# Optimization experiments

Measured on AMD Instinct MI355X. Metric: run time of the kernel, lower is better.

Reference implementation:

```python
import jax, jax.numpy as jnp
from jax import lax
import numpy as np

# db4 (Daubechies-4) filters, matching pywt.Wavelet('db4')
L = 8
_REC_LO = np.array([0.23037781330885523, 0.7148465705525415, 0.6308807679295904,
                    -0.02798376941698385, -0.18703481171888114, 0.030841381835986965,
                    0.032883011666982945, -0.010597401784997278], dtype=np.float32)
_DEC_LO = _REC_LO[::-1].copy()
_DEC_HI = (((-1.0) ** (np.arange(L) + 1)) * _REC_LO).astype(np.float32)  # QMF
_REC_HI = _DEC_HI[::-1].copy()
# lax.conv performs correlation, so use reversed filters to get true convolution.
# rev(dec_lo)=rec_lo, rev(dec_hi)=rec_hi and vice versa.
DEC_K = jnp.asarray(np.stack([_DEC_LO[::-1], _DEC_HI[::-1]])[:, None, :])  # (2,1,L)
REC_K = jnp.asarray(np.stack([_REC_LO[::-1], _REC_HI[::-1]])[None, :, :])  # (1,2,L)

ENHANCE_FACTOR = 1.5
DENOISE_THRESHOLD = 0.2


def _dwt_last(x):
    # pywt single-level DWT (mode='symmetric') along last axis.
    # Equivalent to: conv(sym_pad(x, L-1), dec_filter)[valid][1::2]
    xe = jnp.pad(x, ((0, 0), (L - 1, L - 1)), mode='symmetric')[:, 1:]
    y = lax.conv_general_dilated(xe[:, None, :], DEC_K, (2,), 'VALID',
                                 dimension_numbers=('NCH', 'OIH', 'NCH'))
    return y[:, 0], y[:, 1]  # lo, hi, each (M, (S+L-1)//2)


def _idwt_last(lo, hi):
    # pywt single-level IDWT: upsample (lhs_dilation=2), filter, trim L-2 each side.
    c = jnp.stack([lo, hi], axis=1)  # (M, 2, n)
    y = lax.conv_general_dilated(c, REC_K, (1,), [(1, 1)], lhs_dilation=(2,),
                                 dimension_numbers=('NCH', 'OIH', 'NCH'))
    return y[:, 0]  # (M, 2n - L + 2)


def _dwt2(x):
    # x: (N, H, W) -> aa (cA), da (cH), ad (cV), dd (cD)
    N, H, W = x.shape
    lo, hi = _dwt_last(x.reshape(N * H, W))
    Wc = lo.shape[-1]
    lo = lo.reshape(N, H, Wc)
    hi = hi.reshape(N, H, Wc)

    def colwise(a):
        at = a.transpose(0, 2, 1).reshape(N * Wc, H)
        l, h = _dwt_last(at)
        Hc = l.shape[-1]
        return (l.reshape(N, Wc, Hc).transpose(0, 2, 1),
                h.reshape(N, Wc, Hc).transpose(0, 2, 1))

    aa, da = colwise(lo)
    ad, dd = colwise(hi)
    return aa, da, ad, dd


def _idwt2(aa, da, ad, dd):
    N, Hc, Wc = aa.shape

    def colinv(a, d):
        at = a.transpose(0, 2, 1).reshape(N * Wc, Hc)
        dt = d.transpose(0, 2, 1).reshape(N * Wc, Hc)
        r = _idwt_last(at, dt)
        H = r.shape[-1]
        return r.reshape(N, Wc, H).transpose(0, 2, 1)

    lo = colinv(aa, da)
    hi = colinv(ad, dd)
    H = lo.shape[1]
    out = _idwt_last(lo.reshape(N * H, Wc), hi.reshape(N * H, Wc))
    return out.reshape(N, H, -1)


def _soft_enhance(d):
    # enhance then pywt.threshold(..., mode='soft') with per-(image,channel,band) max
    d = d * ENHANCE_FACTOR
    t = DENOISE_THRESHOLD * jnp.max(jnp.abs(d), axis=(-2, -1), keepdims=True)
    return jnp.sign(d) * jnp.maximum(jnp.abs(d) - t, 0.0)


def setup_inputs() -> dict:
    key = jax.random.key(0)
    x = jax.random.normal(key, (32, 3, 510, 510), dtype=jnp.float32)
    return {'x': x}


def reference(x):
    B, C, H, W = x.shape
    z = x.reshape(B * C, H, W)
    a1, h1, v1, d1 = _dwt2(z)
    a2, h2, v2, d2 = _dwt2(a1)
    h2s, v2s, d2s = _soft_enhance(h2), _soft_enhance(v2), _soft_enhance(d2)
    h1s, v1s, d1s = _soft_enhance(h1), _soft_enhance(v1), _soft_enhance(d1)
    a1r = _idwt2(a2, h2s, v2s, d2s)
    out = _idwt2(a1r, h1s, v1s, d1s)
    return out.reshape(B, C, H, W)
```

## Files before the change

kernel.cpp:

```cpp
#include <hip/hip_runtime.h>

__constant__ float c_dec_lo[8] = {
    -0.010597401784997278f, 0.032883011666982945f, 0.030841381835986965f,
    -0.18703481171888114f, -0.02798376941698385f, 0.6308807679295904f,
    0.7148465705525415f, 0.23037781330885523f};
__constant__ float c_dec_hi[8] = {
    -0.23037781330885523f, 0.7148465705525415f, -0.6308807679295904f,
    -0.02798376941698385f, 0.18703481171888114f, 0.030841381835986965f,
    -0.032883011666982945f, -0.010597401784997278f};
__constant__ float c_rec_lo[8] = {
    0.23037781330885523f, 0.7148465705525415f, 0.6308807679295904f,
    -0.02798376941698385f, -0.18703481171888114f, 0.030841381835986965f,
    0.032883011666982945f, -0.010597401784997278f};
__constant__ float c_rec_hi[8] = {
    -0.010597401784997278f, -0.032883011666982945f, 0.030841381835986965f,
    0.18703481171888114f, -0.02798376941698385f, -0.6308807679295904f,
    0.7148465705525415f, -0.23037781330885523f};

__device__ __forceinline__ float soft_enh(float v, float th) {
    float e = 1.5f * v;
    float a = fabsf(e) - th;
    return a > 0.0f ? copysignf(a, e) : 0.0f;
}

#define TB 32
#define TO 64

__global__ __launch_bounds__(256, 8) void fused_dwt2_k(
    const float* __restrict__ x, int S, int Nc, int tiles,
    float* __restrict__ aa, float* __restrict__ da,
    float* __restrict__ ad, float* __restrict__ dd,
    unsigned* __restrict__ mx_da, unsigned* __restrict__ mx_ad,
    unsigned* __restrict__ mx_dd)
{
    int b = blockIdx.x;
    int tx = b % tiles, ty = (b / tiles) % tiles, m = b / (tiles * tiles);
    int jh0 = ty * TB, jw0 = tx * TB;
    int r0 = 2 * jh0 - 6, c0 = 2 * jw0 - 6;
    const float* xm = x + (size_t)m * S * S;

    __shared__ float RB[70][68];

    int tid = threadIdx.x;
    bool colv = (c0 >= 0) && (c0 + 71 < S);

    if (colv) {
        for (int e = tid; e < 560; e += 256) {
            int r = e >> 3, q = e & 7;
            int pr = r0 + r;
            pr = pr < 0 ? -1 - pr : pr;
            pr = pr >= S ? 2 * S - 1 - pr : pr;
            const float* src = xm + (size_t)pr * S + (c0 + 8 * q);
            float f[16];
#pragma unroll
            for (int i = 0; i < 8; ++i) {
                float2 v = *reinterpret_cast<const float2*>(src + 2 * i);
                f[2 * i] = v.x; f[2 * i + 1] = v.y;
            }
            float lo[4], hi[4];
#pragma unroll
            for (int i = 0; i < 4; ++i) {
                float alo = 0.f, ahi = 0.f;
#pragma unroll
                for (int t = 0; t < 8; ++t) {
                    float v = f[2 * i + 7 - t];
                    alo = fmaf(c_dec_lo[t], v, alo);
                    ahi = fmaf(c_dec_hi[t], v, ahi);
                }
                lo[i] = alo; hi[i] = ahi;
            }
            int c4 = 4 * q;
            *reinterpret_cast<float4*>(&RB[r][c4]) = make_float4(lo[0], lo[1], lo[2], lo[3]);
            *reinterpret_cast<float4*>(&RB[r][32 + c4]) = make_float4(hi[0], hi[1], hi[2], hi[3]);
        }
    } else {
        for (int e = tid; e < 70 * 32; e += 256) {
            int r = e >> 5, jj = e & 31;
            int pr = r0 + r;
            pr = pr < 0 ? -1 - pr : pr;
            pr = pr >= S ? 2 * S - 1 - pr : pr;
            const float* row = xm + (size_t)pr * S;
            int pb = c0 + 2 * jj;
            float alo = 0.f, ahi = 0.f;
#pragma unroll
            for (int t = 0; t < 8; ++t) {
                int p = pb + 7 - t;
                p = p < 0 ? -1 - p : p;
                p = p >= S ? 2 * S - 1 - p : p;
                float v = row[p];
                alo = fmaf(c_dec_lo[t], v, alo);
                ahi = fmaf(c_dec_hi[t], v, ahi);
            }
            RB[r][jj] = alo; RB[r][32 + jj] = ahi;
        }
    }
    __syncthreads();

    int jj = tid & 31, g = tid >> 5;
    int jw = jw0 + jj;
    float mh = 0.f, mv = 0.f, md = 0.f;
#pragma unroll
    for (int pass = 0; pass < 2; ++pass) {
        int rbase = 8 * g + 4 * pass;
        float L[10], H[10];
#pragma unroll
        for (int rr = 0; rr < 10; ++rr) {
            L[rr] = RB[rbase + rr][jj];
            H[rr] = RB[rbase + rr][32 + jj];
        }
#pragma unroll
        for (int k = 0; k < 2; ++k) {
            float vaa = 0.f, vda = 0.f, vad = 0.f, vdd = 0.f;
#pragma unroll
            for (int t = 0; t < 8; ++t) {
                float l = L[2 * k + 7 - t];
                float h = H[2 * k + 7 - t];
                vaa = fmaf(c_dec_lo[t], l, vaa);
                vda = fmaf(c_dec_hi[t], l, vda);
                vad = fmaf(c_dec_lo[t], h, vad);
                vdd = fmaf(c_dec_hi[t], h, vdd);
            }
            int jh = jh0 + 4 * g + 2 * pass + k;
            if (jh < Nc && jw < Nc) {
                size_t o = ((size_t)m * Nc + jh) * Nc + jw;
                aa[o] = vaa; da[o] = vda; ad[o] = vad; dd[o] = vdd;
                mh = fmaxf(mh, fabsf(vda));
                mv = fmaxf(mv, fabsf(vad));
                md = fmaxf(md, fabsf(vdd));
            }
        }
    }
#pragma unroll
    for (int off = 32; off; off >>= 1) {
        mh = fmaxf(mh, __shfl_down(mh, off));
        mv = fmaxf(mv, __shfl_down(mv, off));
        md = fmaxf(md, __shfl_down(md, off));
    }
    __shared__ float sm[3][4];
    int wv = tid >> 6, ln = tid & 63;
    if (ln == 0) { sm[0][wv] = mh; sm[1][wv] = mv; sm[2][wv] = md; }
    __syncthreads();
    if (tid == 0) {
        float A = fmaxf(fmaxf(sm[0][0], sm[0][1]), fmaxf(sm[0][2], sm[0][3]));
        float B = fmaxf(fmaxf(sm[1][0], sm[1][1]), fmaxf(sm[1][2], sm[1][3]));
        float C = fmaxf(fmaxf(sm[2][0], sm[2][1]), fmaxf(sm[2][2], sm[2][3]));
        atomicMax(mx_da + m, __float_as_uint(A));
        atomicMax(mx_ad + m, __float_as_uint(B));
        atomicMax(mx_dd + m, __float_as_uint(C));
    }
}

__global__ __launch_bounds__(256, 8) void fused_idwt2_k(
    const float* __restrict__ a, const float* __restrict__ h,
    const float* __restrict__ v, const float* __restrict__ d,
    const unsigned* __restrict__ mxh, const unsigned* __restrict__ mxv,
    const unsigned* __restrict__ mxd,
    int n, int Ho, int tiles, float* __restrict__ out)
{
    int b = blockIdx.x;
    int tx = b % tiles, ty = (b / tiles) % tiles, m = b / (tiles * tiles);
    int i0 = ty * TO, u0 = tx * TO;
    int jr0 = i0 >> 1, jc0 = u0 >> 1;

    __shared__ float LH[TO][71];

    int tid = threadIdx.x;
    float th_h = 0.2f * (1.5f * __uint_as_float(mxh[m]));
    float th_v = 0.2f * (1.5f * __uint_as_float(mxv[m]));
    float th_d = 0.2f * (1.5f * __uint_as_float(mxd[m]));
    const float* am = a + (size_t)m * n * n;
    const float* hm = h + (size_t)m * n * n;
    const float* vm = v + (size_t)m * n * n;
    const float* dm = d + (size_t)m * n * n;

    for (int task = tid; task < 8 * 35; task += 256) {
        int g = task / 35, jc = task % 35;
        int jcg = jc0 + jc; if (jcg > n - 1) jcg = n - 1;
#pragma unroll
        for (int pass = 0; pass < 2; ++pass) {
            int P = 2 * g + pass;
            float acc_lo[4], acc_hi[4];
#pragma unroll
            for (int k = 0; k < 4; ++k) { acc_lo[k] = 0.f; acc_hi[k] = 0.f; }
#pragma unroll
            for (int rl = 0; rl < 5; ++rl) {
                int jr = jr0 + 2 * P + rl; if (jr > n - 1) jr = n - 1;
                size_t o = (size_t)jr * n + jcg;
                float av = am[o];
                float hv = soft_enh(hm[o], th_h);
                float vv = soft_enh(vm[o], th_v);
                float dv = soft_enh(dm[o], th_d);
#pragma unroll
                for (int t = 0; t < 8; ++t) {
                    int k = 2 * rl + t - 6;
                    if (k >= 0 && k < 4) {
                        acc_lo[k] = fmaf(c_rec_lo[t], av, fmaf(c_rec_hi[t], hv, acc_lo[k]));
                        acc_hi[k] = fmaf(c_rec_lo[t], vv, fmaf(c_rec_hi[t], dv, acc_hi[k]));
                    }
                }
            }
#pragma unroll
            for (int k = 0; k < 4; ++k) {
                LH[4 * P + k][jc] = acc_lo[k];
                LH[4 * P + k][35 + jc] = acc_hi[k];
            }
        }
    }
    __syncthreads();

    for (int e = tid; e < TO * TO; e += 256) {
        int il = e >> 6, ul = e & 63;
        int t0 = ul & 1;
        float acc = 0.f;
#pragma unroll
        for (int s = 0; s < 4; ++s) {
            int t = t0 + 2 * s;
            int c = (ul + 6 - t) >> 1;
            acc = fmaf(c_rec_lo[t], LH[il][c], acc);
            acc = fmaf(c_rec_hi[t], LH[il][35 + c], acc);
        }
        int gi = i0 + il, gu = u0 + ul;
        if (gi < Ho && gu < Ho)
            out[((size_t)m * Ho + gi) * Ho + gu] = acc;
    }
}

extern "C" void kernel_launch(void* const* d_in, const int* in_sizes, int n_in,
                              void* d_out, int out_size, void* d_ws, size_t ws_size,
                              hipStream_t stream) {
    const float* x = (const float*)d_in[0];
    float* out = (float*)d_out;
    float* ws = (float*)d_ws;

    const int M = 96, S1 = 510, N1 = 258, N2 = 132;
    const long S_l1 = (long)M * N1 * N1;
    const long S_l2 = (long)M * N2 * N2;

    float* aa1 = ws;
    float* h1  = aa1 + S_l1;
    float* v1  = h1 + S_l1;
    float* d1  = v1 + S_l1;
    float* a1r = d1 + S_l1;
    float* a2  = a1r + S_l1;
    float* h2  = a2 + S_l2;
    float* v2  = h2 + S_l2;
    float* d2  = v2 + S_l2;
    unsigned* th = (unsigned*)(d2 + S_l2);

    long need = 5 * S_l1 + 4 * S_l2 + 576;
    if (ws_size < (size_t)need * sizeof(float)) return;

    unsigned *th_h1 = th, *th_v1 = th + 96, *th_d1 = th + 192;
    unsigned *th_h2 = th + 288, *th_v2 = th + 384, *th_d2 = th + 480;

    hipMemsetAsync(th, 0, 576 * sizeof(unsigned), stream);

    fused_dwt2_k<<<9 * 9 * M, 256, 0, stream>>>(x, S1, N1, 9, aa1, h1, v1, d1,
                                                th_h1, th_v1, th_d1);
    fused_dwt2_k<<<5 * 5 * M, 256, 0, stream>>>(aa1, N1, N2, 5, a2, h2, v2, d2,
                                                th_h2, th_v2, th_d2);
    fused_idwt2_k<<<5 * 5 * M, 256, 0, stream>>>(a2, h2, v2, d2, th_h2, th_v2, th_d2,
                                                 N2, N1, 5, a1r);
    fused_idwt2_k<<<8 * 8 * M, 256, 0, stream>>>(a1r, h1, v1, d1, th_h1, th_v1, th_d1,
                                                 N1, S1, 8, out);
}
```

Measured before the change: 360.7 us.

## Batch global loads up front, reuse idwt column rows, use constexpr filters

```diff
diff --git a/kernel.cpp b/kernel.cpp
--- a/kernel.cpp
+++ b/kernel.cpp
@@ -1,18 +1,18 @@
 #include <hip/hip_runtime.h>
 
-__constant__ float c_dec_lo[8] = {
+__device__ constexpr float DEC_LO[8] = {
     -0.010597401784997278f, 0.032883011666982945f, 0.030841381835986965f,
     -0.18703481171888114f, -0.02798376941698385f, 0.6308807679295904f,
     0.7148465705525415f, 0.23037781330885523f};
-__constant__ float c_dec_hi[8] = {
+__device__ constexpr float DEC_HI[8] = {
     -0.23037781330885523f, 0.7148465705525415f, -0.6308807679295904f,
     -0.02798376941698385f, 0.18703481171888114f, 0.030841381835986965f,
     -0.032883011666982945f, -0.010597401784997278f};
-__constant__ float c_rec_lo[8] = {
+__device__ constexpr float REC_LO[8] = {
     0.23037781330885523f, 0.7148465705525415f, 0.6308807679295904f,
     -0.02798376941698385f, -0.18703481171888114f, 0.030841381835986965f,
     0.032883011666982945f, -0.010597401784997278f};
-__constant__ float c_rec_hi[8] = {
+__device__ constexpr float REC_HI[8] = {
     -0.010597401784997278f, -0.032883011666982945f, 0.030841381835986965f,
     0.18703481171888114f, -0.02798376941698385f, -0.6308807679295904f,
     0.7148465705525415f, -0.23037781330885523f};
@@ -26,7 +26,7 @@
 #define TB 32
 #define TO 64
 
-__global__ __launch_bounds__(256, 8) void fused_dwt2_k(
+__global__ __launch_bounds__(256, 4) void fused_dwt2_k(
     const float* __restrict__ x, int S, int Nc, int tiles,
     float* __restrict__ aa, float* __restrict__ da,
     float* __restrict__ ad, float* __restrict__ dd,
@@ -44,56 +44,75 @@
     int tid = threadIdx.x;
     bool colv = (c0 >= 0) && (c0 + 71 < S);
 
+    int e0 = tid, e1 = tid + 256, e2 = tid + 512;
+    bool has2 = (e2 < 560);
+
+    auto prow = [&](int e) -> const float* {
+        int pr = r0 + (e >> 3);
+        pr = pr < 0 ? -1 - pr : pr;
+        pr = pr >= S ? 2 * S - 1 - pr : pr;
+        return xm + (size_t)pr * S;
+    };
+
+    float f0[16], f1[16], f2[16];
     if (colv) {
-        for (int e = tid; e < 560; e += 256) {
-            int r = e >> 3, q = e & 7;
-            int pr = r0 + r;
-            pr = pr < 0 ? -1 - pr : pr;
-            pr = pr >= S ? 2 * S - 1 - pr : pr;
-            const float* src = xm + (size_t)pr * S + (c0 + 8 * q);
-            float f[16];
+        const float* s0 = prow(e0) + (c0 + 8 * (e0 & 7));
+        const float* s1 = prow(e1) + (c0 + 8 * (e1 & 7));
+#pragma unroll
+        for (int i = 0; i < 8; ++i) {
+            float2 v = *reinterpret_cast<const float2*>(s0 + 2 * i);
+            f0[2 * i] = v.x; f0[2 * i + 1] = v.y;
+        }
+#pragma unroll
+        for (int i = 0; i < 8; ++i) {
+            float2 v = *reinterpret_cast<const float2*>(s1 + 2 * i);
+            f1[2 * i] = v.x; f1[2 * i + 1] = v.y;
+        }
+        if (has2) {
+            const float* s2 = prow(e2) + (c0 + 8 * (e2 & 7));
 #pragma unroll
             for (int i = 0; i < 8; ++i) {
-                float2 v = *reinterpret_cast<const float2*>(src + 2 * i);
-                f[2 * i] = v.x; f[2 * i + 1] = v.y;
-            }
-            float lo[4], hi[4];
-#pragma unroll
-            for (int i = 0; i < 4; ++i) {
-                float alo = 0.f, ahi = 0.f;
-#pragma unroll
-                for (int t = 0; t < 8; ++t) {
-                    float v = f[2 * i + 7 - t];
-                    alo = fmaf(c_dec_lo[t], v, alo);
-                    ahi = fmaf(c_dec_hi[t], v, ahi);
-                }
-                lo[i] = alo; hi[i] = ahi;
-            }
-            int c4 = 4 * q;
-            *reinterpret_cast<float4*>(&RB[r][c4]) = make_float4(lo[0], lo[1], lo[2], lo[3]);
-            *reinterpret_cast<float4*>(&RB[r][32 + c4]) = make_float4(hi[0], hi[1], hi[2], hi[3]);
+                float2 v = *reinterpret_cast<const float2*>(s2 + 2 * i);
+                f2[2 * i] = v.x; f2[2 * i + 1] = v.y;
+            }
         }
     } else {
-        for (int e = tid; e < 70 * 32; e += 256) {
-            int r = e >> 5, jj = e & 31;
-            int pr = r0 + r;
-            pr = pr < 0 ? -1 - pr : pr;
-            pr = pr >= S ? 2 * S - 1 - pr : pr;
-            const float* row = xm + (size_t)pr * S;
-            int pb = c0 + 2 * jj;
-            float alo = 0.f, ahi = 0.f;
-#pragma unroll
-            for (int t = 0; t < 8; ++t) {
-                int p = pb + 7 - t;
+        auto gath = [&](int e, float* f) {
+            const float* row = prow(e);
+            int base = c0 + 8 * (e & 7);
+#pragma unroll
+            for (int i = 0; i < 16; ++i) {
+                int p = base + i;
                 p = p < 0 ? -1 - p : p;
                 p = p >= S ? 2 * S - 1 - p : p;
-                float v = row[p];
-                alo = fmaf(c_dec_lo[t], v, alo);
-                ahi = fmaf(c_dec_hi[t], v, ahi);
-            }
-            RB[r][jj] = alo; RB[r][32 + jj] = ahi;
-        }
-    }
+                f[i] = row[p];
+            }
+        };
+        gath(e0, f0);
+        gath(e1, f1);
+        if (has2) gath(e2, f2);
+    }
+
+    auto rdwt = [&](int e, const float* f) {
+        float lo[4], hi[4];
+#pragma unroll
+        for (int i = 0; i < 4; ++i) {
+            float alo = 0.f, ahi = 0.f;
+#pragma unroll
+            for (int t = 0; t < 8; ++t) {
+                float v = f[2 * i + 7 - t];
+                alo = fmaf(DEC_LO[t], v, alo);
+                ahi = fmaf(DEC_HI[t], v, ahi);
+            }
+            lo[i] = alo; hi[i] = ahi;
+        }
+        int r = e >> 3, c4 = 4 * (e & 7);
+        *reinterpret_cast<float4*>(&RB[r][c4]) = make_float4(lo[0], lo[1], lo[2], lo[3]);
+        *reinterpret_cast<float4*>(&RB[r][32 + c4]) = make_float4(hi[0], hi[1], hi[2], hi[3]);
+    };
+    rdwt(e0, f0);
+    rdwt(e1, f1);
+    if (has2) rdwt(e2, f2);
     __syncthreads();
 
     int jj = tid & 31, g = tid >> 5;
@@ -115,10 +134,10 @@
             for (int t = 0; t < 8; ++t) {
                 float l = L[2 * k + 7 - t];
                 float h = H[2 * k + 7 - t];
-                vaa = fmaf(c_dec_lo[t], l, vaa);
-                vda = fmaf(c_dec_hi[t], l, vda);
-                vad = fmaf(c_dec_lo[t], h, vad);
-                vdd = fmaf(c_dec_hi[t], h, vdd);
+                vaa = fmaf(DEC_LO[t], l, vaa);
+                vda = fmaf(DEC_HI[t], l, vda);
+                vad = fmaf(DEC_LO[t], h, vad);
+                vdd = fmaf(DEC_HI[t], h, vdd);
             }
             int jh = jh0 + 4 * g + 2 * pass + k;
             if (jh < Nc && jw < Nc) {
@@ -150,7 +169,7 @@
     }
 }
 
-__global__ __launch_bounds__(256, 8) void fused_idwt2_k(
+__global__ __launch_bounds__(256, 4) void fused_idwt2_k(
     const float* __restrict__ a, const float* __restrict__ h,
     const float* __restrict__ v, const float* __restrict__ d,
     const unsigned* __restrict__ mxh, const unsigned* __restrict__ mxv,
@@ -173,9 +192,25 @@
     const float* vm = v + (size_t)m * n * n;
     const float* dm = d + (size_t)m * n * n;
 
-    for (int task = tid; task < 8 * 35; task += 256) {
+    auto coltask = [&](int task) {
         int g = task / 35, jc = task % 35;
         int jcg = jc0 + jc; if (jcg > n - 1) jcg = n - 1;
+        float Ar[7], Hr[7], Vr[7], Dr[7];
+#pragma unroll
+        for (int rr = 0; rr < 7; ++rr) {
+            int jr = jr0 + 4 * g + rr; if (jr > n - 1) jr = n - 1;
+            size_t o = (size_t)jr * n + jcg;
+            Ar[rr] = am[o];
+            Hr[rr] = hm[o];
+            Vr[rr] = vm[o];
+            Dr[rr] = dm[o];
+        }
+#pragma unroll
+        for (int rr = 0; rr < 7; ++rr) {
+            Hr[rr] = soft_enh(Hr[rr], th_h);
+            Vr[rr] = soft_enh(Vr[rr], th_v);
+            Dr[rr] = soft_enh(Dr[rr], th_d);
+        }
 #pragma unroll
         for (int pass = 0; pass < 2; ++pass) {
             int P = 2 * g + pass;
@@ -184,18 +219,14 @@
             for (int k = 0; k < 4; ++k) { acc_lo[k] = 0.f; acc_hi[k] = 0.f; }
 #pragma unroll
             for (int rl = 0; rl < 5; ++rl) {
-                int jr = jr0 + 2 * P + rl; if (jr > n - 1) jr = n - 1;
-                size_t o = (size_t)jr * n + jcg;
-                float av = am[o];
-                float hv = soft_enh(hm[o], th_h);
-                float vv = soft_enh(vm[o], th_v);
-                float dv = soft_enh(dm[o], th_d);
+                int rr = 2 * pass + rl;
+                float av = Ar[rr], hv = Hr[rr], vv = Vr[rr], dv = Dr[rr];
 #pragma unroll
                 for (int t = 0; t < 8; ++t) {
                     int k = 2 * rl + t - 6;
                     if (k >= 0 && k < 4) {
-                        acc_lo[k] = fmaf(c_rec_lo[t], av, fmaf(c_rec_hi[t], hv, acc_lo[k]));
-                        acc_hi[k] = fmaf(c_rec_lo[t], vv, fmaf(c_rec_hi[t], dv, acc_hi[k]));
+                        acc_lo[k] = fmaf(REC_LO[t], av, fmaf(REC_HI[t], hv, acc_lo[k]));
+                        acc_hi[k] = fmaf(REC_LO[t], vv, fmaf(REC_HI[t], dv, acc_hi[k]));
                     }
                 }
             }
@@ -205,7 +236,9 @@
                 LH[4 * P + k][35 + jc] = acc_hi[k];
             }
         }
-    }
+    };
+    coltask(tid);
+    if (tid + 256 < 8 * 35) coltask(tid + 256);
     __syncthreads();
 
     for (int e = tid; e < TO * TO; e += 256) {
@@ -216,8 +249,8 @@
         for (int s = 0; s < 4; ++s) {
             int t = t0 + 2 * s;
             int c = (ul + 6 - t) >> 1;
-            acc = fmaf(c_rec_lo[t], LH[il][c], acc);
-            acc = fmaf(c_rec_hi[t], LH[il][35 + c], acc);
+            acc = fmaf(REC_LO[t], LH[il][c], acc);
+            acc = fmaf(REC_HI[t], LH[il][35 + c], acc);
         }
         int gi = i0 + il, gu = u0 + ul;
         if (gi < Ho && gu < Ho)
```

Result: faster. 337.1 us (-6.5%).
